# Kernel optimization log

Measured on AMD Instinct MI355X. Metric: run time of the kernel, lower is better.

## Reference

```python
import jax, jax.numpy as jnp
import numpy as np


def gcn_conv(x, W, b, src, dst, num_nodes):
    # PyG GCNConv: h = D^{-1/2} (A + I) D^{-1/2} (x W) + b
    h = x @ W  # [N, H]
    ones = jnp.ones(src.shape[0], dtype=h.dtype)
    deg = jax.ops.segment_sum(ones, dst, num_segments=num_nodes) + 1.0  # +1 for self-loop
    d_inv_sqrt = jax.lax.rsqrt(deg)
    norm = d_inv_sqrt[src] * d_inv_sqrt[dst]  # [E]
    msg = h[src] * norm[:, None]  # [E, H] gather
    agg = jax.ops.segment_sum(msg, dst, num_segments=num_nodes)  # scatter-add
    agg = agg + h * (1.0 / deg)[:, None]  # self-loop term: deg_i^{-1/2} * deg_i^{-1/2}
    return agg + b


def setup_inputs() -> dict:
    key = jax.random.key(0)
    ks = jax.random.split(key, 10)
    N, E, F, H, C, G = 100000, 1000000, 64, 128, 2, 512
    x = jax.random.normal(ks[0], (N, F), dtype=jnp.float32)
    edge_index = jax.random.randint(ks[1], (2, E), 0, N, dtype=jnp.int64)
    batch = jnp.sort(jax.random.randint(ks[2], (N,), 0, G, dtype=jnp.int64))
    s1 = 1.0 / np.sqrt(F)
    s2 = 1.0 / np.sqrt(H)
    W1 = jax.random.normal(ks[3], (F, H), dtype=jnp.float32) * s1
    b1 = jnp.zeros((H,), dtype=jnp.float32)
    W2 = jax.random.normal(ks[4], (H, H), dtype=jnp.float32) * s2
    b2 = jnp.zeros((H,), dtype=jnp.float32)
    Wfc = jax.random.normal(ks[5], (H, C), dtype=jnp.float32) * s2
    bfc = jnp.zeros((C,), dtype=jnp.float32)
    return {"x": x, "edge_index": edge_index, "batch": batch, "num_graphs": G,
            "W1": W1, "b1": b1, "W2": W2, "b2": b2, "Wfc": Wfc, "bfc": bfc}


def reference(x, edge_index, batch, num_graphs, W1, b1, W2, b2, Wfc, bfc):
    # Dropout is inference-mode (identity), matching model.eval().
    N = x.shape[0]
    src, dst = edge_index[0], edge_index[1]
    h = gcn_conv(x, W1, b1, src, dst, N)
    h = jax.nn.relu(h)
    h = gcn_conv(h, W2, b2, src, dst, N)
    h = jax.nn.relu(h)
    # global mean pool over graphs
    summed = jax.ops.segment_sum(h, batch, num_segments=num_graphs)  # [G, H]
    counts = jax.ops.segment_sum(jnp.ones((N,), h.dtype), batch, num_segments=num_graphs)
    pooled = summed / jnp.maximum(counts, 1.0)[:, None]
    logits = pooled @ Wfc + bfc  # [G, C]
    return jax.nn.softmax(logits, axis=1)
```

## Files before the change

kernel.cpp:

```cpp
#include <hip/hip_runtime.h>
#include <hip/hip_bf16.h>

typedef __hip_bfloat16 bf16;
typedef __attribute__((ext_vector_type(8))) short short8;
typedef __attribute__((ext_vector_type(4))) float f32x4;
typedef __attribute__((ext_vector_type(2))) float f32x2;

#define FDIM 64
#define HDIM 128

#define ESTRIDE 4096
#define EC 8192
#define ECPT (EC / 256)

__device__ __forceinline__ float b2f(bf16 v) { return __bfloat162float(v); }
__device__ __forceinline__ float bits2f(unsigned int u) {
    return __uint_as_float(u << 16);
}
__device__ __forceinline__ unsigned short f2bits(float f) {
    bf16 b = __float2bfloat16(f);
    return *reinterpret_cast<unsigned short*>(&b);
}
__device__ __forceinline__ unsigned char f2fp8(float v) {
    int pk = __builtin_amdgcn_cvt_pk_fp8_f32(v, v, 0, false);
    return (unsigned char)(pk & 0xFF);
}

__global__ __launch_bounds__(256) void k_prep_flags(const unsigned short* __restrict__ w1u,
                                                    const int* __restrict__ edge,
                                                    const int* __restrict__ batch,
                                                    int* __restrict__ flags,
                                                    int* __restrict__ zbase, int zn4) {
    if (blockIdx.x == 0 && threadIdx.x < 192) {
        int wave = threadIdx.x >> 6, lane = threadIdx.x & 63;
        if (wave == 0) {
            int wild = 0;
#pragma unroll
            for (int r = 0; r < 2; r++) {
                int i = 2 * lane + 128 * r;
                int e = (w1u[i] >> 7) & 0xFF;
                wild += (e == 0 || e >= 137) ? 1 : 0;
            }
            for (int s = 32; s; s >>= 1) wild += __shfl_down(wild, s);
            if (lane == 0) flags[0] = (wild > 16) ? 1 : 0;
        } else if (wave == 1) {
            int z = 0;
#pragma unroll
            for (int r = 0; r < 2; r++) {
                int i = 2 * lane + 1 + 128 * r;
                z += (edge[i] == 0) ? 1 : 0;
            }
            for (int s = 32; s; s >>= 1) z += __shfl_down(z, s);
            if (lane == 0) flags[1] = (z > 64) ? 1 : 0;
        } else {
            int z = 0;
#pragma unroll
            for (int r = 0; r < 2; r++) {
                int i = 1025 + 2 * lane + 128 * r;
                z += (batch[i] == 0) ? 1 : 0;
            }
            for (int s = 32; s; s >>= 1) z += __shfl_down(z, s);
            if (lane == 0) flags[2] = (z > 64) ? 1 : 0;
        }
    }
    int4 zz = make_int4(0, 0, 0, 0);
    int stride = gridDim.x * 256;
    for (int t = blockIdx.x * 256 + threadIdx.x; t < zn4; t += stride)
        ((int4*)zbase)[t] = zz;
}

__device__ __forceinline__ int edge_word(const int* e, long long logical_idx, int is64) {
    return is64 ? e[2 * logical_idx] : e[logical_idx];
}

__global__ __launch_bounds__(256) void k_phase1(const int* __restrict__ edge,
                                                int* __restrict__ gcur,
                                                int* __restrict__ ebuf,
                                                int E,
                                                const void* __restrict__ W1, const void* __restrict__ b1,
                                                const void* __restrict__ W2, const void* __restrict__ b2,
                                                const void* __restrict__ Wfc, const void* __restrict__ bfc,
                                                bf16* __restrict__ W1t, bf16* __restrict__ W2t,
                                                bf16* __restrict__ b1c, bf16* __restrict__ b2c,
                                                bf16* __restrict__ Wfcc, bf16* __restrict__ bfcc,
                                                const void* __restrict__ x,
                                                unsigned char* __restrict__ X8,
                                                int totalX4, const int* __restrict__ flags,
                                                const int* __restrict__ batch,
                                                int* __restrict__ gstart,
                                                int N, int G,
                                                int NB1, int WB, int XB) {
    int blk = blockIdx.x;
    if (blk < NB1) {
        __shared__ int h[512];
        int tid = threadIdx.x;
        for (int b2 = tid; b2 < 512; b2 += 256) h[b2] = 0;
        __syncthreads();
        int is64 = flags[1];
        int e0 = blk * EC;
        int dcache[ECPT];
#pragma unroll
        for (int k = 0; k < ECPT; k++) {
            int i = e0 + (k << 8) + tid;
            int d = -1;
            if (i < E) d = edge_word(edge, (long long)E + i, is64);
            dcache[k] = d;
            if (d >= 0) atomicAdd(&h[(d >> 8) & 511], 1);
        }
        __syncthreads();
        for (int b2 = tid; b2 < 512; b2 += 256) {
            int c = h[b2];
            h[b2] = c ? atomicAdd(&gcur[b2], c) : 0;
        }
        __syncthreads();
#pragma unroll
        for (int k = 0; k < ECPT; k++) {
            int i = e0 + (k << 8) + tid;
            int d = dcache[k];
            if (d >= 0) {
                int s = edge_word(edge, i, is64);
                int bb = (d >> 8) & 511;
                int pos = atomicAdd(&h[bb], 1);
                if ((unsigned)pos < (unsigned)ESTRIDE)
                    ebuf[(bb << 12) + pos] = s | ((d & 255) << 24);
            }
        }
    } else if (blk < NB1 + WB) {
        int f0 = flags[0];
        int gid = (blk - NB1) * 256 + threadIdx.x;
        int stride = WB * 256;
#define CV(src, si) (f0 ? __float2bfloat16(((const float*)(src))[si]) : ((const bf16*)(src))[si])
        for (int i = gid; i < FDIM * HDIM; i += stride) {
            int n = i >> 6, k = i & 63;
            W1t[i] = CV(W1, k * HDIM + n);
        }
        for (int i = gid; i < HDIM * HDIM; i += stride) {
            int n = i >> 7, k = i & 127;
            W2t[i] = CV(W2, k * HDIM + n);
        }
        for (int i = gid; i < HDIM; i += stride) b1c[i] = CV(b1, i);
        for (int i = gid; i < HDIM; i += stride) b2c[i] = CV(b2, i);
        for (int i = gid; i < HDIM * 2; i += stride) Wfcc[i] = CV(Wfc, i);
        for (int i = gid; i < 2; i += stride) bfcc[i] = CV(bfc, i);
#undef CV
    } else if (blk < NB1 + WB + XB) {
        int t = (blk - NB1 - WB) * 256 + threadIdx.x;
        if (t >= totalX4) return;
        float4 v;
        if (flags[0]) {
            v = ((const float4*)x)[t];
        } else {
            uint2 p = ((const uint2*)x)[t];
            v.x = bits2f(p.x & 0xFFFFu); v.y = bits2f(p.x >> 16);
            v.z = bits2f(p.y & 0xFFFFu); v.w = bits2f(p.y >> 16);
        }
        unsigned int q0 = (unsigned int)__builtin_amdgcn_cvt_pk_fp8_f32(v.x, v.y, 0, false) & 0xFFFFu;
        unsigned int q1 = (unsigned int)__builtin_amdgcn_cvt_pk_fp8_f32(v.z, v.w, 0, false) & 0xFFFFu;
        ((unsigned int*)X8)[t] = (q1 << 16) | q0;
    } else {
        int i = (blk - NB1 - WB - XB) * 256 + threadIdx.x;
        if (i >= N) return;
        int is64 = flags[2];
        int bi = is64 ? batch[2 * i] : batch[i];
        if (i == 0) {
            for (int g = 0; g <= bi; g++) gstart[g] = 0;
        } else {
            int bp = is64 ? batch[2 * (i - 1)] : batch[i - 1];
            for (int g = bp + 1; g <= bi; g++) gstart[g] = i;
        }
        if (i == N - 1) {
            for (int g = bi + 1; g <= G; g++) gstart[g] = N;
        }
    }
}

__global__ __launch_bounds__(256) void k_csr(const int* __restrict__ ebuf,
                                             const int* __restrict__ gcur,
                                             int* __restrict__ rowptr,
                                             int* __restrict__ cnt,
                                             float* __restrict__ dinv,
                                             int* __restrict__ srclist,
                                             int N) {
    __shared__ int sred[256];
    __shared__ int sc[256];
    __shared__ int sa[256], sb[256];
    int b = blockIdx.x;
    int tid = threadIdx.x;
    int part = 0;
    for (int j = tid; j < b; j += 256) {
        int v = gcur[j];
        part += (v > ESTRIDE) ? ESTRIDE : v;
    }
    sred[tid] = part;
    __syncthreads();
    for (int s = 128; s > 0; s >>= 1) {
        if (tid < s) sred[tid] += sred[tid + s];
        __syncthreads();
    }
    int gbase = sred[0];
    int cnt_b = gcur[b];
    if (cnt_b > ESTRIDE) cnt_b = ESTRIDE;
    sc[tid] = 0;
    __syncthreads();
    const int* eb = ebuf + (b << 12);
    for (int j = tid; j < cnt_b; j += 256) {
        int p = eb[j];
        atomicAdd(&sc[(unsigned)p >> 24], 1);
    }
    __syncthreads();
    int cval = sc[tid];
    sa[tid] = cval;
    __syncthreads();
    int* cur = sa; int* nxt = sb;
    for (int off = 1; off < 256; off <<= 1) {
        int v = cur[tid];
        if (tid >= off) v += cur[tid - off];
        nxt[tid] = v;
        __syncthreads();
        int* t = cur; cur = nxt; nxt = t;
    }
    int excl = cur[tid] - cval;
    int node = (b << 8) + tid;
    if (node < N) {
        rowptr[node] = gbase + excl;
        cnt[node] = cval;
        dinv[node] = rsqrtf((float)cval + 1.0f);
    }
    __syncthreads();
    sc[tid] = excl;
    __syncthreads();
    for (int j = tid; j < cnt_b; j += 256) {
        int p = eb[j];
        int pos = atomicAdd(&sc[(unsigned)p >> 24], 1);
        srclist[gbase + pos] = p & 0xFFFFFF;
    }
}

#define ACCFP8(u2, e) do { \
    f32x2 f01 = __builtin_amdgcn_cvt_pk_f32_fp8((u2).x, false); \
    f32x2 f23 = __builtin_amdgcn_cvt_pk_f32_fp8((u2).x, true); \
    f32x2 f45 = __builtin_amdgcn_cvt_pk_f32_fp8((u2).y, false); \
    f32x2 f67 = __builtin_amdgcn_cvt_pk_f32_fp8((u2).y, true); \
    acc[0] += f01[0] * (e); acc[1] += f01[1] * (e); \
    acc[2] += f23[0] * (e); acc[3] += f23[1] * (e); \
    acc[4] += f45[0] * (e); acc[5] += f45[1] * (e); \
    acc[6] += f67[0] * (e); acc[7] += f67[1] * (e); } while (0)

#define K1PAD 72
__global__ __launch_bounds__(256) void k_agg_gemmA(const unsigned char* __restrict__ x8,
                                                   const int* __restrict__ srclist,
                                                   const int* __restrict__ rowptr,
                                                   const int* __restrict__ count,
                                                   const float* __restrict__ dinv,
                                                   const bf16* __restrict__ W1t,
                                                   const bf16* __restrict__ bias,
                                                   unsigned char* __restrict__ h8, int N) {
    __shared__ bf16 As[64 * K1PAD];
    __shared__ bf16 Wt[HDIM * K1PAD];
    __shared__ float bsf[HDIM];
    int tid = threadIdx.x;
    int base = blockIdx.x * 64;
    {
        const uint4* wsrc = (const uint4*)W1t;
        for (int i = tid; i < HDIM * 8; i += 256) {
            int n = i >> 3, c = i & 7;
            *(uint4*)&Wt[n * K1PAD + c * 8] = wsrc[n * 8 + c];
        }
    }
    if (tid < HDIM) bsf[tid] = b2f(bias[tid]);
    int wave = tid >> 6, lane = tid & 63;
    int group = lane >> 3, sub = lane & 7, lb = group << 3;
    const uint2* hrow = (const uint2*)x8;
#pragma unroll
    for (int pass = 0; pass < 2; pass++) {
        int r = pass * 32 + wave * 8 + group;
        int i = base + r;
        float acc[8] = {0.f, 0.f, 0.f, 0.f, 0.f, 0.f, 0.f, 0.f};
        if (i < N) {
            int start = rowptr[i];
            int cnt = count[i];
            float di = dinv[i];
            for (int jb = 0; jb < cnt; jb += 8) {
                int m = cnt - jb; if (m > 8) m = 8;
                int sv = srclist[start + jb + ((sub < m) ? sub : (m - 1))];
                float dvv = dinv[sv];
                int j = 0;
                for (; j + 4 <= m; j += 4) {
                    int s0 = __shfl(sv, lb + j + 0); float e0 = __shfl(dvv, lb + j + 0);
                    int s1 = __shfl(sv, lb + j + 1); float e1 = __shfl(dvv, lb + j + 1);
                    int s2 = __shfl(sv, lb + j + 2); float e2 = __shfl(dvv, lb + j + 2);
                    int s3 = __shfl(sv, lb + j + 3); float e3 = __shfl(dvv, lb + j + 3);
                    uint2 v0 = hrow[(size_t)s0 * 8 + sub];
                    uint2 v1 = hrow[(size_t)s1 * 8 + sub];
                    uint2 v2 = hrow[(size_t)s2 * 8 + sub];
                    uint2 v3 = hrow[(size_t)s3 * 8 + sub];
                    ACCFP8(v0, e0); ACCFP8(v1, e1); ACCFP8(v2, e2); ACCFP8(v3, e3);
                }
                for (; j < m; j++) {
                    int s0 = __shfl(sv, lb + j); float e0 = __shfl(dvv, lb + j);
                    uint2 v0 = hrow[(size_t)s0 * 8 + sub];
                    ACCFP8(v0, e0);
                }
            }
            uint2 vs = hrow[(size_t)i * 8 + sub];
            float self = di * di;
            float sacc[8] = {0.f};
            {
                float* acc = sacc;
                ACCFP8(vs, self);
            }
#pragma unroll
            for (int k = 0; k < 8; k++) acc[k] = di * acc[k] + sacc[k];
        }
        uint4 pv;
        pv.x = ((unsigned int)f2bits(acc[1]) << 16) | f2bits(acc[0]);
        pv.y = ((unsigned int)f2bits(acc[3]) << 16) | f2bits(acc[2]);
        pv.z = ((unsigned int)f2bits(acc[5]) << 16) | f2bits(acc[4]);
        pv.w = ((unsigned int)f2bits(acc[7]) << 16) | f2bits(acc[6]);
        *(uint4*)&As[r * K1PAD + sub * 8] = pv;
    }
    __syncthreads();
    int l15 = lane & 15, q = lane >> 4;
    int m0 = wave * 16;
    short8 af[2];
#pragma unroll
    for (int kc = 0; kc < 2; kc++)
        af[kc] = *(const short8*)&As[(m0 + l15) * K1PAD + kc * 32 + q * 8];
    f32x4 acc[8];
#pragma unroll
    for (int nt = 0; nt < 8; nt++) {
        acc[nt] = (f32x4){0.f, 0.f, 0.f, 0.f};
#pragma unroll
        for (int kc = 0; kc < 2; kc++) {
            short8 bf = *(const short8*)&Wt[(nt * 16 + l15) * K1PAD + kc * 32 + q * 8];
            acc[nt] = __builtin_amdgcn_mfma_f32_16x16x32_bf16(af[kc], bf, acc[nt], 0, 0, 0);
        }
    }
#pragma unroll
    for (int nt = 0; nt < 8; nt++) {
        int col = nt * 16 + l15;
        float bv = bsf[col];
#pragma unroll
        for (int r = 0; r < 4; r++) {
            int gr = base + m0 + q * 4 + r;
            if (gr < N) {
                float v = fmaxf(acc[nt][r] + bv, 0.f);
                h8[(size_t)gr * HDIM + col] = f2fp8(v);
            }
        }
    }
}

#define K2PAD 136
__global__ __launch_bounds__(256) void k_agg_gemmB(const unsigned char* __restrict__ h8,
                                                   const int* __restrict__ srclist,
                                                   const int* __restrict__ rowptr,
                                                   const int* __restrict__ count,
                                                   const float* __restrict__ dinv,
                                                   const bf16* __restrict__ W2t,
                                                   const bf16* __restrict__ bias,
                                                   bf16* __restrict__ outp, int N) {
    __shared__ bf16 As[64 * K2PAD];
    __shared__ bf16 Wt[HDIM * K2PAD];
    __shared__ float bsf[HDIM];
    int tid = threadIdx.x;
    int base = blockIdx.x * 64;
    {
        const uint4* wsrc = (const uint4*)W2t;
        for (int i = tid; i < HDIM * 16; i += 256) {
            int n = i >> 4, c = i & 15;
            *(uint4*)&Wt[n * K2PAD + c * 8] = wsrc[n * 16 + c];
        }
    }
    if (tid < HDIM) bsf[tid] = b2f(bias[tid]);
    int wave = tid >> 6, lane = tid & 63;
    int group = lane >> 4, sub = lane & 15, lb = group << 4;
    const uint2* hrow = (const uint2*)h8;
#pragma unroll
    for (int pass = 0; pass < 4; pass++) {
        int r = pass * 16 + wave * 4 + group;
        int i = base + r;
        float acc[8] = {0.f, 0.f, 0.f, 0.f, 0.f, 0.f, 0.f, 0.f};
        if (i < N) {
            int start = rowptr[i];
            int cnt = count[i];
            float di = dinv[i];
            for (int jb = 0; jb < cnt; jb += 16) {
                int m = cnt - jb; if (m > 16) m = 16;
                int sv = srclist[start + jb + ((sub < m) ? sub : (m - 1))];
                float dvv = dinv[sv];
                int j = 0;
                for (; j + 4 <= m; j += 4) {
                    int s0 = __shfl(sv, lb + j + 0); float e0 = __shfl(dvv, lb + j + 0);
                    int s1 = __shfl(sv, lb + j + 1); float e1 = __shfl(dvv, lb + j + 1);
                    int s2 = __shfl(sv, lb + j + 2); float e2 = __shfl(dvv, lb + j + 2);
                    int s3 = __shfl(sv, lb + j + 3); float e3 = __shfl(dvv, lb + j + 3);
                    uint2 v0 = hrow[(size_t)s0 * 16 + sub];
                    uint2 v1 = hrow[(size_t)s1 * 16 + sub];
                    uint2 v2 = hrow[(size_t)s2 * 16 + sub];
                    uint2 v3 = hrow[(size_t)s3 * 16 + sub];
                    ACCFP8(v0, e0); ACCFP8(v1, e1); ACCFP8(v2, e2); ACCFP8(v3, e3);
                }
                for (; j < m; j++) {
                    int s0 = __shfl(sv, lb + j); float e0 = __shfl(dvv, lb + j);
                    uint2 v0 = hrow[(size_t)s0 * 16 + sub];
                    ACCFP8(v0, e0);
                }
            }
            uint2 vs = hrow[(size_t)i * 16 + sub];
            float self = di * di;
            float sacc[8] = {0.f};
            {
                float* acc = sacc;
                ACCFP8(vs, self);
            }
#pragma unroll
            for (int k = 0; k < 8; k++) acc[k] = di * acc[k] + sacc[k];
        }
        uint4 pv;
        pv.x = ((unsigned int)f2bits(acc[1]) << 16) | f2bits(acc[0]);
        pv.y = ((unsigned int)f2bits(acc[3]) << 16) | f2bits(acc[2]);
        pv.z = ((unsigned int)f2bits(acc[5]) << 16) | f2bits(acc[4]);
        pv.w = ((unsigned int)f2bits(acc[7]) << 16) | f2bits(acc[6]);
        *(uint4*)&As[r * K2PAD + sub * 8] = pv;
    }
    __syncthreads();
    int l15 = lane & 15, q = lane >> 4;
    int m0 = wave * 16;
    short8 af[4];
#pragma unroll
    for (int kc = 0; kc < 4; kc++)
        af[kc] = *(const short8*)&As[(m0 + l15) * K2PAD + kc * 32 + q * 8];
    f32x4 acc[8];
#pragma unroll
    for (int nt = 0; nt < 8; nt++) {
        acc[nt] = (f32x4){0.f, 0.f, 0.f, 0.f};
#pragma unroll
        for (int kc = 0; kc < 4; kc++) {
            short8 bf = *(const short8*)&Wt[(nt * 16 + l15) * K2PAD + kc * 32 + q * 8];
            acc[nt] = __builtin_amdgcn_mfma_f32_16x16x32_bf16(af[kc], bf, acc[nt], 0, 0, 0);
        }
    }
#pragma unroll
    for (int nt = 0; nt < 8; nt++) {
        int col = nt * 16 + l15;
        float bv = bsf[col];
#pragma unroll
        for (int r = 0; r < 4; r++) {
            int gr = base + m0 + q * 4 + r;
            if (gr < N) outp[(size_t)gr * HDIM + col] = __float2bfloat16(fmaxf(acc[nt][r] + bv, 0.f));
        }
    }
}

__global__ __launch_bounds__(256) void k_pool(const bf16* __restrict__ hact,
                                              const int* __restrict__ gstart,
                                              const bf16* __restrict__ Wfc,
                                              const bf16* __restrict__ bfc,
                                              void* __restrict__ out,
                                              const int* __restrict__ flags) {
    __shared__ float lds[16][HDIM + 1];
    __shared__ float colsum[HDIM];
    int g = blockIdx.x;
    int s = gstart[g], e = gstart[g + 1];
    int tid = threadIdx.x;
    int cslot = tid & 15;
    int rslot = tid >> 4;
    const uint4* hp = (const uint4*)hact;
    float a[8] = {0.f, 0.f, 0.f, 0.f, 0.f, 0.f, 0.f, 0.f};
    for (int r = s + rslot; r < e; r += 16) {
        uint4 v = hp[(size_t)r * 16 + cslot];
        a[0] += bits2f(v.x & 0xFFFFu); a[1] += bits2f(v.x >> 16);
        a[2] += bits2f(v.y & 0xFFFFu); a[3] += bits2f(v.y >> 16);
        a[4] += bits2f(v.z & 0xFFFFu); a[5] += bits2f(v.z >> 16);
        a[6] += bits2f(v.w & 0xFFFFu); a[7] += bits2f(v.w >> 16);
    }
#pragma unroll
    for (int k = 0; k < 8; k++) lds[rslot][cslot * 8 + k] = a[k];
    __syncthreads();
    if (tid < HDIM) {
        float sum = 0.f;
#pragma unroll
        for (int k = 0; k < 16; k++) sum += lds[k][tid];
        colsum[tid] = sum;
    }
    __syncthreads();
    if (tid >= 64) return;
    int lane = tid;
    float inv = 1.0f / fmaxf((float)(e - s), 1.0f);
    float m0 = colsum[2 * lane] * inv;
    float m1 = colsum[2 * lane + 1] * inv;
    float l0 = m0 * b2f(Wfc[(2 * lane) * 2 + 0]) + m1 * b2f(Wfc[(2 * lane + 1) * 2 + 0]);
    float l1 = m0 * b2f(Wfc[(2 * lane) * 2 + 1]) + m1 * b2f(Wfc[(2 * lane + 1) * 2 + 1]);
    for (int sft = 32; sft; sft >>= 1) { l0 += __shfl_down(l0, sft); l1 += __shfl_down(l1, sft); }
    if (lane == 0) {
        float z0 = l0 + b2f(bfc[0]);
        float z1 = l1 + b2f(bfc[1]);
        float mx = fmaxf(z0, z1);
        float e0 = expf(z0 - mx), e1 = expf(z1 - mx);
        float sm = e0 + e1;
        float p0 = e0 / sm, p1 = e1 / sm;
        if (flags[0]) {
            ((float*)out)[2 * g + 0] = p0;
            ((float*)out)[2 * g + 1] = p1;
        } else {
            ((bf16*)out)[2 * g + 0] = __float2bfloat16(p0);
            ((bf16*)out)[2 * g + 1] = __float2bfloat16(p1);
        }
    }
}

extern "C" void kernel_launch(void* const* d_in, const int* in_sizes, int n_in,
                              void* d_out, int out_size, void* d_ws, size_t ws_size,
                              hipStream_t stream) {
    const void* x    = d_in[0];
    const int*  edge = (const int*)d_in[1];
    const int*  batch= (const int*)d_in[2];
    const void* W1  = d_in[4];
    const void* b1  = d_in[5];
    const void* W2  = d_in[6];
    const void* b2  = d_in[7];
    const void* Wfc = d_in[8];
    const void* bfc = d_in[9];

    int N = in_sizes[0] / FDIM;
    int E = in_sizes[1] / 2;
    int G = out_size / 2;

    int*   flags  = (int*)d_ws;
    float* dinv   = (float*)((char*)d_ws + 64);
    int*   gcur   = (int*)(dinv + N);
    int*   gstart = gcur + 512;
    int*   rowptr = gstart + 516;
    int*   count  = rowptr + N;
    int*   srclist= count + N;
    int*   ebuf   = srclist + E;
    bf16*  Bbuf   = (bf16*)(ebuf + 512 * ESTRIDE);
    bf16*  b1c    = Bbuf + (size_t)N * HDIM;
    bf16*  b2c    = b1c + HDIM;
    bf16*  Wfcc   = b2c + HDIM;
    bf16*  bfcc   = Wfcc + 256;
    bf16*  W1t    = bfcc + 64;
    bf16*  W2t    = W1t + FDIM * HDIM;
    unsigned char* H8 = (unsigned char*)(W2t + HDIM * HDIM);
    unsigned char* X8 = H8 + (size_t)N * HDIM;

    int NB  = (N + 255) >> 8;
    int NB1 = (E + EC - 1) / EC;
    int WB = 32;
    int XB = (N * 16 + 255) / 256;
    int BB = (N + 255) / 256;
    int totalX4 = N * 16;
    int zn4 = 512 / 4;

    k_prep_flags<<<4, 256, 0, stream>>>((const unsigned short*)W1, edge, batch, flags,
                                        gcur, zn4);
    k_phase1<<<NB1 + WB + XB + BB, 256, 0, stream>>>(edge, gcur, ebuf, E,
                                                     W1, b1, W2, b2, Wfc, bfc,
                                                     W1t, W2t, b1c, b2c, Wfcc, bfcc,
                                                     x, X8, totalX4, flags,
                                                     batch, gstart, N, G,
                                                     NB1, WB, XB);
    k_csr<<<NB, 256, 0, stream>>>(ebuf, gcur, rowptr, count, dinv, srclist, N);

    k_agg_gemmA<<<(N + 63) / 64, 256, 0, stream>>>(X8, srclist, rowptr, count, dinv,
                                                   W1t, b1c, H8, N);
    k_agg_gemmB<<<(N + 63) / 64, 256, 0, stream>>>(H8, srclist, rowptr, count, dinv,
                                                   W2t, b2c, Bbuf, N);

    k_pool<<<G, 256, 0, stream>>>(Bbuf, gstart, Wfcc, bfcc, d_out, flags);
}
```

Before: 233.9 us.

## Split layer-2 aggregation from GEMM into separate kernels and unroll gathers by 8

Layer-2 aggregation now runs as its own kernel with 16 rows per block (more blocks, no large shared-memory footprint), and writes bf16 results to a new intermediate buffer. A separate GEMM kernel then loads those rows from global memory into LDS and does the MFMA. Both aggregation paths gain an 8-wide unrolled gather that issues more independent loads at once. The cost is an extra N×128 bf16 round trip through global memory and one more kernel launch.

```diff
diff --git a/kernel.cpp b/kernel.cpp
--- a/kernel.cpp
+++ b/kernel.cpp
@@ -284,22 +284,32 @@
                 int m = cnt - jb; if (m > 8) m = 8;
                 int sv = srclist[start + jb + ((sub < m) ? sub : (m - 1))];
                 float dvv = dinv[sv];
-                int j = 0;
-                for (; j + 4 <= m; j += 4) {
-                    int s0 = __shfl(sv, lb + j + 0); float e0 = __shfl(dvv, lb + j + 0);
-                    int s1 = __shfl(sv, lb + j + 1); float e1 = __shfl(dvv, lb + j + 1);
-                    int s2 = __shfl(sv, lb + j + 2); float e2 = __shfl(dvv, lb + j + 2);
-                    int s3 = __shfl(sv, lb + j + 3); float e3 = __shfl(dvv, lb + j + 3);
-                    uint2 v0 = hrow[(size_t)s0 * 8 + sub];
-                    uint2 v1 = hrow[(size_t)s1 * 8 + sub];
-                    uint2 v2 = hrow[(size_t)s2 * 8 + sub];
-                    uint2 v3 = hrow[(size_t)s3 * 8 + sub];
-                    ACCFP8(v0, e0); ACCFP8(v1, e1); ACCFP8(v2, e2); ACCFP8(v3, e3);
-                }
-                for (; j < m; j++) {
-                    int s0 = __shfl(sv, lb + j); float e0 = __shfl(dvv, lb + j);
-                    uint2 v0 = hrow[(size_t)s0 * 8 + sub];
-                    ACCFP8(v0, e0);
+                if (m == 8) {
+                    int s[8]; float e[8]; uint2 v[8];
+#pragma unroll
+                    for (int t = 0; t < 8; t++) { s[t] = __shfl(sv, lb + t); e[t] = __shfl(dvv, lb + t); }
+#pragma unroll
+                    for (int t = 0; t < 8; t++) v[t] = hrow[(size_t)s[t] * 8 + sub];
+#pragma unroll
+                    for (int t = 0; t < 8; t++) ACCFP8(v[t], e[t]);
+                } else {
+                    int j = 0;
+                    for (; j + 4 <= m; j += 4) {
+                        int s0 = __shfl(sv, lb + j + 0); float e0 = __shfl(dvv, lb + j + 0);
+                        int s1 = __shfl(sv, lb + j + 1); float e1 = __shfl(dvv, lb + j + 1);
+                        int s2 = __shfl(sv, lb + j + 2); float e2 = __shfl(dvv, lb + j + 2);
+                        int s3 = __shfl(sv, lb + j + 3); float e3 = __shfl(dvv, lb + j + 3);
+                        uint2 v0 = hrow[(size_t)s0 * 8 + sub];
+                        uint2 v1 = hrow[(size_t)s1 * 8 + sub];
+                        uint2 v2 = hrow[(size_t)s2 * 8 + sub];
+                        uint2 v3 = hrow[(size_t)s3 * 8 + sub];
+                        ACCFP8(v0, e0); ACCFP8(v1, e1); ACCFP8(v2, e2); ACCFP8(v3, e3);
+                    }
+                    for (; j < m; j++) {
+                        int s0 = __shfl(sv, lb + j); float e0 = __shfl(dvv, lb + j);
+                        uint2 v0 = hrow[(size_t)s0 * 8 + sub];
+                        ACCFP8(v0, e0);
+                    }
                 }
             }
             uint2 vs = hrow[(size_t)i * 8 + sub];
@@ -351,15 +361,79 @@
     }
 }
 
+__global__ __launch_bounds__(256) void k_agg128(const unsigned char* __restrict__ h8,
+                                                const int* __restrict__ srclist,
+                                                const int* __restrict__ rowptr,
+                                                const int* __restrict__ count,
+                                                const float* __restrict__ dinv,
+                                                bf16* __restrict__ outb, int N) {
+    int wave = threadIdx.x >> 6;
+    int lane = threadIdx.x & 63;
+    int group = lane >> 4;
+    int sub = lane & 15;
+    int i = blockIdx.x * 16 + wave * 4 + group;
+    if (i >= N) return;
+    int start = rowptr[i];
+    int cnt = count[i];
+    float di = dinv[i];
+    const uint2* hrow = (const uint2*)h8;
+    float acc[8] = {0.f, 0.f, 0.f, 0.f, 0.f, 0.f, 0.f, 0.f};
+    int lb = group << 4;
+    for (int jb = 0; jb < cnt; jb += 16) {
+        int m = cnt - jb; if (m > 16) m = 16;
+        int sv = srclist[start + jb + ((sub < m) ? sub : (m - 1))];
+        float dvv = dinv[sv];
+        int j = 0;
+        for (; j + 8 <= m; j += 8) {
+            int s[8]; float e[8]; uint2 v[8];
+#pragma unroll
+            for (int t = 0; t < 8; t++) { s[t] = __shfl(sv, lb + j + t); e[t] = __shfl(dvv, lb + j + t); }
+#pragma unroll
+            for (int t = 0; t < 8; t++) v[t] = hrow[(size_t)s[t] * 16 + sub];
+#pragma unroll
+            for (int t = 0; t < 8; t++) ACCFP8(v[t], e[t]);
+        }
+        for (; j + 4 <= m; j += 4) {
+            int s0 = __shfl(sv, lb + j + 0); float e0 = __shfl(dvv, lb + j + 0);
+            int s1 = __shfl(sv, lb + j + 1); float e1 = __shfl(dvv, lb + j + 1);
+            int s2 = __shfl(sv, lb + j + 2); float e2 = __shfl(dvv, lb + j + 2);
+            int s3 = __shfl(sv, lb + j + 3); float e3 = __shfl(dvv, lb + j + 3);
+            uint2 v0 = hrow[(size_t)s0 * 16 + sub];
+            uint2 v1 = hrow[(size_t)s1 * 16 + sub];
+            uint2 v2 = hrow[(size_t)s2 * 16 + sub];
+            uint2 v3 = hrow[(size_t)s3 * 16 + sub];
+            ACCFP8(v0, e0); ACCFP8(v1, e1); ACCFP8(v2, e2); ACCFP8(v3, e3);
+        }
+        for (; j < m; j++) {
+            int s0 = __shfl(sv, lb + j); float e0 = __shfl(dvv, lb + j);
+            uint2 v0 = hrow[(size_t)s0 * 16 + sub];
+            ACCFP8(v0, e0);
+        }
+    }
+    {
+        uint2 vs = hrow[(size_t)i * 16 + sub];
+        float self = di * di;
+        float sacc[8] = {0.f};
+        {
+            float* acc = sacc;
+            ACCFP8(vs, self);
+        }
+#pragma unroll
+        for (int k = 0; k < 8; k++) acc[k] = di * acc[k] + sacc[k];
+    }
+    uint4 pv;
+    pv.x = ((unsigned int)f2bits(acc[1]) << 16) | f2bits(acc[0]);
+    pv.y = ((unsigned int)f2bits(acc[3]) << 16) | f2bits(acc[2]);
+    pv.z = ((unsigned int)f2bits(acc[5]) << 16) | f2bits(acc[4]);
+    pv.w = ((unsigned int)f2bits(acc[7]) << 16) | f2bits(acc[6]);
+    ((uint4*)outb)[(size_t)i * 16 + sub] = pv;
+}
+
 #define K2PAD 136
-__global__ __launch_bounds__(256) void k_agg_gemmB(const unsigned char* __restrict__ h8,
-                                                   const int* __restrict__ srclist,
-                                                   const int* __restrict__ rowptr,
-                                                   const int* __restrict__ count,
-                                                   const float* __restrict__ dinv,
-                                                   const bf16* __restrict__ W2t,
-                                                   const bf16* __restrict__ bias,
-                                                   bf16* __restrict__ outp, int N) {
+__global__ __launch_bounds__(256) void k_gemmB(const bf16* __restrict__ Z,
+                                               const bf16* __restrict__ W2t,
+                                               const bf16* __restrict__ bias,
+                                               bf16* __restrict__ outp, int N) {
     __shared__ bf16 As[64 * K2PAD];
     __shared__ bf16 Wt[HDIM * K2PAD];
     __shared__ float bsf[HDIM];
@@ -372,61 +446,17 @@
             *(uint4*)&Wt[n * K2PAD + c * 8] = wsrc[n * 16 + c];
         }
     }
+    const uint4* xb = (const uint4*)Z;
+    for (int i = tid; i < 64 * 16; i += 256) {
+        int r = i >> 4, c = i & 15;
+        int gr = base + r; if (gr >= N) gr = N - 1;
+        *(uint4*)&As[r * K2PAD + c * 8] = xb[(size_t)gr * 16 + c];
+    }
     if (tid < HDIM) bsf[tid] = b2f(bias[tid]);
-    int wave = tid >> 6, lane = tid & 63;
-    int group = lane >> 4, sub = lane & 15, lb = group << 4;
-    const uint2* hrow = (const uint2*)h8;
-#pragma unroll
-    for (int pass = 0; pass < 4; pass++) {
-        int r = pass * 16 + wave * 4 + group;
-        int i = base + r;
-        float acc[8] = {0.f, 0.f, 0.f, 0.f, 0.f, 0.f, 0.f, 0.f};
-        if (i < N) {
-            int start = rowptr[i];
-            int cnt = count[i];
-            float di = dinv[i];
-            for (int jb = 0; jb < cnt; jb += 16) {
-                int m = cnt - jb; if (m > 16) m = 16;
-                int sv = srclist[start + jb + ((sub < m) ? sub : (m - 1))];
-                float dvv = dinv[sv];
-                int j = 0;
-                for (; j + 4 <= m; j += 4) {
-                    int s0 = __shfl(sv, lb + j + 0); float e0 = __shfl(dvv, lb + j + 0);
-                    int s1 = __shfl(sv, lb + j + 1); float e1 = __shfl(dvv, lb + j + 1);
-                    int s2 = __shfl(sv, lb + j + 2); float e2 = __shfl(dvv, lb + j + 2);
-                    int s3 = __shfl(sv, lb + j + 3); float e3 = __shfl(dvv, lb + j + 3);
-                    uint2 v0 = hrow[(size_t)s0 * 16 + sub];
-                    uint2 v1 = hrow[(size_t)s1 * 16 + sub];
-                    uint2 v2 = hrow[(size_t)s2 * 16 + sub];
-                    uint2 v3 = hrow[(size_t)s3 * 16 + sub];
-                    ACCFP8(v0, e0); ACCFP8(v1, e1); ACCFP8(v2, e2); ACCFP8(v3, e3);
-                }
-                for (; j < m; j++) {
-                    int s0 = __shfl(sv, lb + j); float e0 = __shfl(dvv, lb + j);
-                    uint2 v0 = hrow[(size_t)s0 * 16 + sub];
-                    ACCFP8(v0, e0);
-                }
-            }
-            uint2 vs = hrow[(size_t)i * 16 + sub];
-            float self = di * di;
-            float sacc[8] = {0.f};
-            {
-                float* acc = sacc;
-                ACCFP8(vs, self);
-            }
-#pragma unroll
-            for (int k = 0; k < 8; k++) acc[k] = di * acc[k] + sacc[k];
-        }
-        uint4 pv;
-        pv.x = ((unsigned int)f2bits(acc[1]) << 16) | f2bits(acc[0]);
-        pv.y = ((unsigned int)f2bits(acc[3]) << 16) | f2bits(acc[2]);
-        pv.z = ((unsigned int)f2bits(acc[5]) << 16) | f2bits(acc[4]);
-        pv.w = ((unsigned int)f2bits(acc[7]) << 16) | f2bits(acc[6]);
-        *(uint4*)&As[r * K2PAD + sub * 8] = pv;
-    }
-    __syncthreads();
+    __syncthreads();
+    int wid = tid >> 6, lane = tid & 63;
     int l15 = lane & 15, q = lane >> 4;
-    int m0 = wave * 16;
+    int m0 = wid * 16;
     short8 af[4];
 #pragma unroll
     for (int kc = 0; kc < 4; kc++)
@@ -535,7 +565,8 @@
     int*   count  = rowptr + N;
     int*   srclist= count + N;
     int*   ebuf   = srclist + E;
-    bf16*  Bbuf   = (bf16*)(ebuf + 512 * ESTRIDE);
+    bf16*  Zbuf   = (bf16*)(ebuf + 512 * ESTRIDE);
+    bf16*  Bbuf   = Zbuf + (size_t)N * HDIM;
     bf16*  b1c    = Bbuf + (size_t)N * HDIM;
     bf16*  b2c    = b1c + HDIM;
     bf16*  Wfcc   = b2c + HDIM;
@@ -565,8 +596,8 @@
 
     k_agg_gemmA<<<(N + 63) / 64, 256, 0, stream>>>(X8, srclist, rowptr, count, dinv,
                                                    W1t, b1c, H8, N);
-    k_agg_gemmB<<<(N + 63) / 64, 256, 0, stream>>>(H8, srclist, rowptr, count, dinv,
-                                                   W2t, b2c, Bbuf, N);
+    k_agg128<<<(N + 15) / 16, 256, 0, stream>>>(H8, srclist, rowptr, count, dinv, Zbuf, N);
+    k_gemmB<<<(N + 63) / 64, 256, 0, stream>>>(Zbuf, W2t, b2c, Bbuf, N);
 
     k_pool<<<G, 256, 0, stream>>>(Bbuf, gstart, Wfcc, bfcc, d_out, flags);
 }
```

New measurement: 238.4 us. Within noise of the previous version (+1.9%).
